# Kernel tuning notes

Hardware: AMD Instinct MI355X
Metric: run time of the kernel (lower is better)

## Reference

```python
import jax, jax.numpy as jnp
import numpy as np

D_MODEL = 1024
NHEAD = 16
HEAD_DIM = D_MODEL // NHEAD
MASK_FILLER = -1e20


def setup_inputs() -> dict:
    key = jax.random.key(0)
    ks = jax.random.split(key, 8)
    B, S = 2, 2048
    query = jax.random.normal(ks[0], (B, S, D_MODEL), dtype=jnp.float32)
    key_t = jax.random.normal(ks[1], (B, S, D_MODEL), dtype=jnp.float32)
    value = jax.random.normal(ks[2], (B, S, D_MODEL), dtype=jnp.float32)
    mask = jax.random.randint(ks[3], (B, S, S), 0, 2, dtype=jnp.int32)
    # nn.Linear(d_model, d_model, bias=False) weights, shape [out, in]
    scale = 1.0 / np.sqrt(D_MODEL)
    wq = jax.random.uniform(ks[4], (D_MODEL, D_MODEL), jnp.float32, -scale, scale)
    wk = jax.random.uniform(ks[5], (D_MODEL, D_MODEL), jnp.float32, -scale, scale)
    wv = jax.random.uniform(ks[6], (D_MODEL, D_MODEL), jnp.float32, -scale, scale)
    wo = jax.random.uniform(ks[7], (D_MODEL, D_MODEL), jnp.float32, -scale, scale)
    return {"query": query, "key": key_t, "value": value, "mask": mask,
            "wq": wq, "wk": wk, "wv": wv, "wo": wo}


def reference(query, key, value, mask, wq, wk, wv, wo):
    B = query.shape[0]
    # Projections: nn.Linear -> x @ W.T
    q = (query @ wq.T).reshape(B, -1, NHEAD, HEAD_DIM).transpose(0, 2, 1, 3)  # [B,H,Sq,Dh]
    k = (key @ wk.T).reshape(B, -1, NHEAD, HEAD_DIM).transpose(0, 2, 1, 3)    # [B,H,Sk,Dh]
    v = (value @ wv.T).reshape(B, -1, NHEAD, HEAD_DIM).transpose(0, 2, 1, 3)  # [B,H,Sk,Dh]
    scores = jnp.einsum('bhqd,bhkd->bhqk', q, k) / jnp.sqrt(jnp.float32(HEAD_DIM))
    scores = jnp.where(mask[:, None, :, :] == 0, MASK_FILLER, scores)
    attn = jax.nn.softmax(scores, axis=-1)  # dropout p=0.0 -> identity
    out = jnp.einsum('bhqk,bhkd->bhqd', attn, v)  # [B,H,Sq,Dh]
    out = out.transpose(0, 2, 1, 3).reshape(B, -1, D_MODEL)
    return out @ wo.T
```

## Files before the change

kernel.cpp:

```cpp
#include <hip/hip_runtime.h>
#include <stdint.h>

typedef __bf16 bf16x8 __attribute__((ext_vector_type(8)));
typedef float floatx4 __attribute__((ext_vector_type(4)));
typedef unsigned short ushort8v __attribute__((ext_vector_type(8)));
typedef unsigned int uint4v __attribute__((ext_vector_type(4)));
typedef unsigned int uint2v __attribute__((ext_vector_type(2)));
typedef unsigned short u16;
typedef unsigned long long u64;

#define GLOAD_LDS16(gp, lp)                                                       \
  __builtin_amdgcn_global_load_lds((__attribute__((address_space(1))) void*)(gp), \
                                   (__attribute__((address_space(3))) void*)(lp), \
                                   16, 0, 0)

__device__ __forceinline__ u16 f2bf(float f) {
  uint32_t u = __builtin_bit_cast(uint32_t, f);
  u = (u + 0x7FFFu + ((u >> 16) & 1u)) >> 16;
  return (u16)u;
}
__device__ __forceinline__ u16 f2bf_up(float f) {
  return (u16)((__builtin_bit_cast(uint32_t, f) + 0x8000u) >> 16);
}

__device__ __forceinline__ ushort8v load8(const void* base, size_t elemOff, int isf32) {
  if (isf32) {
    const uint32_t* p = (const uint32_t*)base + elemOff;
    uint4v a = *(const uint4v*)p;
    uint4v b = *(const uint4v*)(p + 4);
#pragma unroll
    for (int i = 0; i < 4; ++i) { a[i] += 0x8000u; b[i] += 0x8000u; }
    uint4v r;
    r[0] = __builtin_amdgcn_perm(a[1], a[0], 0x07060302);
    r[1] = __builtin_amdgcn_perm(a[3], a[2], 0x07060302);
    r[2] = __builtin_amdgcn_perm(b[1], b[0], 0x07060302);
    r[3] = __builtin_amdgcn_perm(b[3], b[2], 0x07060302);
    return __builtin_bit_cast(ushort8v, r);
  }
  return *(const ushort8v*)((const u16*)base + elemOff);
}

__global__ void detect_dtype(const u16* __restrict__ q, int* __restrict__ flag) {
  if (threadIdx.x == 0) *flag = 0;
  __syncthreads();
  int hit = 0;
  for (int i = threadIdx.x; i < 8192; i += 256) {
    u16 u = q[i];
    if (((u >> 7) & 0xFF) == 0xFF) hit = 1;
  }
  if (hit) atomicOr(flag, 1);
}

__global__ void pack_mask(const int* __restrict__ mask, u64* __restrict__ mpk) {
  const int gw   = (blockIdx.x * 256 + threadIdx.x) >> 6;
  const int lane = threadIdx.x & 63;
  const int word = gw & 31;
  const int row  = gw >> 5;
  const int m = mask[(size_t)row * 2048 + word * 64 + lane];
  u64 bits = __ballot(m != 0);
  if (lane == 0) mpk[(size_t)row * 32 + word] = bits;
}

__global__ __launch_bounds__(256)
void cvt_all(const void* X0, const void* X1, const void* X2,
             const void* W0, const void* W1, const void* W2, const void* W3,
             u16* __restrict__ Xb, u16* __restrict__ Wb, const int* flagp)
{
  const int isf = *flagp;
  const int id = blockIdx.x;
  const int t  = threadIdx.x;
  const int r2  = t >> 7;
  const int col = (t & 127) * 8;
  const void* src; u16* dst; int row;
  if (id < 6144) {
    const int s = id >> 11;
    src = (s == 0) ? X0 : (s == 1) ? X1 : X2;
    row = (id & 2047) * 2 + r2;
    dst = Xb + (size_t)s * 4096 * 1040 + (size_t)row * 1040 + col;
  } else {
    const int s = (id - 6144) >> 9;
    src = (s == 0) ? W0 : (s == 1) ? W1 : (s == 2) ? W2 : W3;
    row = ((id - 6144) & 511) * 2 + r2;
    dst = Wb + (size_t)s * 1024 * 1040 + (size_t)row * 1040 + col;
  }
  *(ushort8v*)dst = load8(src, (size_t)row * 1024 + col, isf);
}

__global__ __launch_bounds__(256)
void cvt_w(const void* W0, const void* W1, const void* W2, const void* W3,
           u16* __restrict__ dst, const int* flagp) {
  const int isf = *flagp;
  const int z = blockIdx.y;
  const void* src = (z == 0) ? W0 : (z == 1) ? W1 : (z == 2) ? W2 : W3;
  const size_t off = ((size_t)blockIdx.x * 256 + threadIdx.x) * 8;
  *(ushort8v*)(dst + (size_t)z * 1024 * 1024 + off) = load8(src, off, isf);
}

__global__ __launch_bounds__(256, 3)
void gemm_qkv_b(const u16* __restrict__ Xb, const u16* __restrict__ Wb,
                u16* __restrict__ Qb, u16* __restrict__ Kb, u16* __restrict__ Vt)
{
  const int AS = 1040, WS = 1040, N = 1024, K = 1024;
  const int z = blockIdx.z;
  const u16* A = Xb + (size_t)z * 4096 * AS;
  const u16* W = Wb + (size_t)z * 1024 * WS;

  __shared__ __align__(16) u16 lA[2 * 128 * 32];
  __shared__ __align__(16) u16 lB[2 * 128 * 32];

  const int tid  = threadIdx.x;
  const int lane = tid & 63;
  const int quad = lane >> 4;
  const int l15  = lane & 15;
  const int w    = tid >> 6;
  const int wm   = w >> 1, wn = w & 1;
  const int tileM = blockIdx.x * 128;
  const int tileN = blockIdx.y * 128;

  floatx4 acc[4][4] = {};

  const int ldRow = tid >> 2;
  const int ldCol = (tid & 3) * 8;
  const u16* aG = A + (size_t)(tileM + ldRow) * AS + ldCol;
  const u16* bG = W + (size_t)(tileN + ldRow) * WS + ldCol;
  u16* lAp = lA + tid * 8;
  u16* lBp = lB + tid * 8;

  GLOAD_LDS16(aG, lAp);
  GLOAD_LDS16(aG + (size_t)64 * AS, lAp + 2048);
  GLOAD_LDS16(bG, lBp);
  GLOAD_LDS16(bG + (size_t)64 * WS, lBp + 2048);
  __syncthreads();

#pragma unroll 2
  for (int k0 = 0; k0 < K; k0 += 32) {
    const int cur = (k0 >> 5) & 1;
    const int nxo = 4096 * (cur ^ 1);
    if (k0 + 32 < K) {
      GLOAD_LDS16(aG + k0 + 32, lAp + nxo);
      GLOAD_LDS16(aG + (size_t)64 * AS + k0 + 32, lAp + nxo + 2048);
      GLOAD_LDS16(bG + k0 + 32, lBp + nxo);
      GLOAD_LDS16(bG + (size_t)64 * WS + k0 + 32, lBp + nxo + 2048);
    }
    const u16* cA = lA + 4096 * cur;
    const u16* cB = lB + 4096 * cur;
    bf16x8 af[4], bw[4];
#pragma unroll
    for (int i = 0; i < 4; ++i) {
      af[i] = *(const bf16x8*)&cA[(wm * 64 + i * 16 + l15) * 32 + quad * 8];
      bw[i] = *(const bf16x8*)&cB[(wn * 64 + i * 16 + l15) * 32 + quad * 8];
    }
#pragma unroll
    for (int i = 0; i < 4; ++i)
#pragma unroll
      for (int j = 0; j < 4; ++j)
        acc[i][j] = __builtin_amdgcn_mfma_f32_16x16x32_bf16(af[i], bw[j], acc[i][j], 0, 0, 0);
    __syncthreads();
  }

  if (z < 2) {
    u16* C = (z == 0) ? Qb : Kb;
    const float sc = (z == 0) ? 0.18033688011112042f : 1.0f;
#pragma unroll
    for (int i = 0; i < 4; ++i) {
      const int row0 = tileM + wm * 64 + i * 16 + quad * 4;
#pragma unroll
      for (int j = 0; j < 4; ++j) {
        const int col = tileN + wn * 64 + j * 16 + l15;
#pragma unroll
        for (int r = 0; r < 4; ++r)
          C[(size_t)(row0 + r) * N + col] = f2bf(acc[i][j][r] * sc);
      }
    }
  } else {
    const int half = w >> 1;
    u16* myT = (w & 1) ? lB : lA;
#pragma unroll
    for (int pass = 0; pass < 2; ++pass) {
      __syncthreads();
      if (half == pass) {
#pragma unroll
        for (int i = 0; i < 4; ++i)
#pragma unroll
          for (int j = 0; j < 4; ++j)
#pragma unroll
            for (int r = 0; r < 4; ++r) {
              const int lr = i * 16 + quad * 4 + r;
              const int lc = j * 16 + l15;
              myT[lr * 64 + (lc ^ (quad << 4))] = f2bf(acc[i][j][r]);
            }
      }
      __syncthreads();
      if (half == pass) {
        const int n    = lane;
        const int gcol = tileN + wn * 64 + n;
        const int hh = gcol >> 6, dd = gcol & 63;
        const int growBase = tileM + wm * 64;
        const int bb = growBase >> 11;
        const int s0 = growBase & 2047;
        u16* dst = Vt + (((size_t)bb * 16 + hh) * 64 + dd) * 2048 + s0;
#pragma unroll
        for (int m0 = 0; m0 < 64; m0 += 8) {
          ushort8v pk;
#pragma unroll
          for (int t = 0; t < 8; ++t) {
            const int m = m0 + t;
            pk[t] = myT[m * 64 + (n ^ ((m & 12) << 2))];
          }
          *(ushort8v*)(dst + m0) = pk;
        }
      }
    }
  }
}

__global__ __launch_bounds__(256)
void gemm_qkv_f(const void* X0, const void* X1, const void* X2,
                const u16* __restrict__ Wb,
                u16* __restrict__ Qb, u16* __restrict__ Kb, u16* __restrict__ Vt,
                const int* flagp)
{
  const int K = 1024, N = 1024;
  const int isf = *flagp;
  const int z = blockIdx.z;
  const void* A_ = (z == 0) ? X0 : (z == 1) ? X1 : X2;
  const u16* W = Wb + (size_t)z * 1024 * 1024;

  __shared__ __align__(16) u16 lA[128 * 32];
  __shared__ __align__(16) u16 lB[128 * 32];

  const int tid  = threadIdx.x;
  const int lane = tid & 63;
  const int quad = lane >> 4;
  const int l15  = lane & 15;
  const int w    = tid >> 6;
  const int wm   = w >> 1, wn = w & 1;
  const int tileM = blockIdx.x * 128;
  const int tileN = blockIdx.y * 128;

  floatx4 acc[4][4] = {};

  const int ldRow = tid >> 2;
  const int ldCol = (tid & 3) * 8;
  const size_t aOff = (size_t)(tileM + ldRow) * K + ldCol;
  const u16* bG = W + (size_t)(tileN + ldRow) * K + ldCol;
  u16* lAp = lA + tid * 8;
  u16* lBp = lB + tid * 8;

  ushort8v a0 = load8(A_, aOff, isf);
  ushort8v a1 = load8(A_, aOff + (size_t)64 * K, isf);
  ushort8v b0 = *(const ushort8v*)bG;
  ushort8v b1 = *(const ushort8v*)(bG + (size_t)64 * K);

  for (int k0 = 0; k0 < K; k0 += 32) {
    __syncthreads();
    *(ushort8v*)lAp          = a0;
    *(ushort8v*)(lAp + 2048) = a1;
    *(ushort8v*)lBp          = b0;
    *(ushort8v*)(lBp + 2048) = b1;
    __syncthreads();

    if (k0 + 32 < K) {
      a0 = load8(A_, aOff + k0 + 32, isf);
      a1 = load8(A_, aOff + (size_t)64 * K + k0 + 32, isf);
      b0 = *(const ushort8v*)(bG + k0 + 32);
      b1 = *(const ushort8v*)(bG + (size_t)64 * K + k0 + 32);
    }

    bf16x8 af[4], bw[4];
#pragma unroll
    for (int i = 0; i < 4; ++i) {
      af[i] = *(const bf16x8*)&lA[(wm * 64 + i * 16 + l15) * 32 + quad * 8];
      bw[i] = *(const bf16x8*)&lB[(wn * 64 + i * 16 + l15) * 32 + quad * 8];
    }
#pragma unroll
    for (int i = 0; i < 4; ++i)
#pragma unroll
      for (int j = 0; j < 4; ++j)
        acc[i][j] = __builtin_amdgcn_mfma_f32_16x16x32_bf16(af[i], bw[j], acc[i][j], 0, 0, 0);
  }

  if (z < 2) {
    u16* C = (z == 0) ? Qb : Kb;
    const float sc = (z == 0) ? 0.18033688011112042f : 1.0f;
#pragma unroll
    for (int i = 0; i < 4; ++i) {
      const int row0 = tileM + wm * 64 + i * 16 + quad * 4;
#pragma unroll
      for (int j = 0; j < 4; ++j) {
        const int col = tileN + wn * 64 + j * 16 + l15;
#pragma unroll
        for (int r = 0; r < 4; ++r)
          C[(size_t)(row0 + r) * N + col] = f2bf(acc[i][j][r] * sc);
      }
    }
  } else {
    const int half = w >> 1;
    u16* myT = (w & 1) ? lB : lA;
#pragma unroll
    for (int pass = 0; pass < 2; ++pass) {
      __syncthreads();
      if (half == pass) {
#pragma unroll
        for (int i = 0; i < 4; ++i)
#pragma unroll
          for (int j = 0; j < 4; ++j)
#pragma unroll
            for (int r = 0; r < 4; ++r) {
              const int lr = i * 16 + quad * 4 + r;
              const int lc = j * 16 + l15;
              myT[lr * 64 + (lc ^ (quad << 4))] = f2bf(acc[i][j][r]);
            }
      }
      __syncthreads();
      if (half == pass) {
        const int n    = lane;
        const int gcol = tileN + wn * 64 + n;
        const int hh = gcol >> 6, dd = gcol & 63;
        const int growBase = tileM + wm * 64;
        const int bb = growBase >> 11;
        const int s0 = growBase & 2047;
        u16* dst = Vt + (((size_t)bb * 16 + hh) * 64 + dd) * 2048 + s0;
#pragma unroll
        for (int m0 = 0; m0 < 64; m0 += 8) {
          ushort8v pk;
#pragma unroll
          for (int t = 0; t < 8; ++t) {
            const int m = m0 + t;
            pk[t] = myT[m * 64 + (n ^ ((m & 12) << 2))];
          }
          *(ushort8v*)(dst + m0) = pk;
        }
      }
    }
  }
}

__global__ __launch_bounds__(256)
void attn(const u16* Qb, const u16* __restrict__ Kb, const u16* __restrict__ Vt,
          const u64* __restrict__ mpk, u16* AO, int aoStr)
{
  __shared__ __align__(16) u16 lK[2][64 * 64];
  __shared__ __align__(16) u16 lV[64 * 64];
  __shared__ __align__(16) u16 lP[4][16 * 64];

  const int tid  = threadIdx.x;
  const int lane = tid & 63;
  const int quad = lane >> 4;
  const int l15  = lane & 15;
  const int w    = tid >> 6;

  const int bh = blockIdx.x;
  const int qt = blockIdx.y;
  const int b  = bh >> 4;
  const int h  = bh & 15;
  const size_t rowB   = (size_t)b * 2048;
  const size_t vtBase = ((size_t)bh * 64) * 2048;

  bf16x8 aq[2];
  {
    const u16* qp = Qb + (rowB + qt * 64 + w * 16 + l15) * 1024 + h * 64 + quad * 8;
    aq[0] = *(const bf16x8*)qp;
    aq[1] = *(const bf16x8*)(qp + 32);
  }

  const ushort8v one_u = {0x3F80, 0x3F80, 0x3F80, 0x3F80, 0x3F80, 0x3F80, 0x3F80, 0x3F80};
  const bf16x8 ones = __builtin_bit_cast(bf16x8, one_u);

  floatx4 o[4], l4;
#pragma unroll
  for (int nb = 0; nb < 4; ++nb) o[nb] = (floatx4){0.f, 0.f, 0.f, 0.f};
  l4 = (floatx4){0.f, 0.f, 0.f, 0.f};

  const u64* mrow = mpk + (rowB + qt * 64 + w * 16 + l15) * 32;
  u16* lPw = &lP[w][0];

  const int r1 = tid >> 3;
  const int cs = ((tid & 7) ^ (r1 & 7)) * 8;
  const u16* kSrc = Kb + (rowB + r1) * 1024 + h * 64 + cs;
  const u16* vSrc = Vt + vtBase + (size_t)r1 * 2048 + cs;

  GLOAD_LDS16(kSrc,                     &lK[0][tid * 8]);
  GLOAD_LDS16(kSrc + (size_t)32 * 1024, &lK[0][tid * 8 + 2048]);

#pragma unroll 2
  for (int kt = 0; kt < 32; ++kt) {
    const int cur = kt & 1;
    __syncthreads();

    {
      const u16* vS = vSrc + kt * 64;
      GLOAD_LDS16(vS,                     &lV[tid * 8]);
      GLOAD_LDS16(vS + (size_t)32 * 2048, &lV[tid * 8 + 2048]);
    }
    if (kt < 31) {
      const u16* kS = kSrc + (size_t)(kt + 1) * 64 * 1024;
      GLOAD_LDS16(kS,                     &lK[cur ^ 1][tid * 8]);
      GLOAD_LDS16(kS + (size_t)32 * 1024, &lK[cur ^ 1][tid * 8 + 2048]);
    }

    const u64 mw = mrow[kt];

#pragma unroll
    for (int nb = 0; nb < 4; ++nb) {
      const int row = nb * 16 + l15;
      const int swk = (row & 7) << 3;
      bf16x8 ak0 = *(const bf16x8*)&lK[cur][row * 64 + ((quad * 8) ^ swk)];
      bf16x8 ak1 = *(const bf16x8*)&lK[cur][row * 64 + ((quad * 8 + 32) ^ swk)];
      floatx4 sacc = {0.f, 0.f, 0.f, 0.f};
      sacc = __builtin_amdgcn_mfma_f32_16x16x32_bf16(ak0, aq[0], sacc, 0, 0, 0);
      sacc = __builtin_amdgcn_mfma_f32_16x16x32_bf16(ak1, aq[1], sacc, 0, 0, 0);
      const uint32_t nib = (uint32_t)(mw >> (nb * 16 + quad * 4)) & 0xFu;
      float p0 = (nib & 1u) ? __builtin_amdgcn_exp2f(sacc[0]) : 0.0f;
      float p1 = (nib & 2u) ? __builtin_amdgcn_exp2f(sacc[1]) : 0.0f;
      float p2 = (nib & 4u) ? __builtin_amdgcn_exp2f(sacc[2]) : 0.0f;
      float p3 = (nib & 8u) ? __builtin_amdgcn_exp2f(sacc[3]) : 0.0f;
      const uint32_t b0 = __builtin_bit_cast(uint32_t, p0) + 0x8000u;
      const uint32_t b1 = __builtin_bit_cast(uint32_t, p1) + 0x8000u;
      const uint32_t b2 = __builtin_bit_cast(uint32_t, p2) + 0x8000u;
      const uint32_t b3 = __builtin_bit_cast(uint32_t, p3) + 0x8000u;
      uint2v pk2;
      pk2[0] = __builtin_amdgcn_perm(b1, b0, 0x07060302);
      pk2[1] = __builtin_amdgcn_perm(b3, b2, 0x07060302);
      const int col = (nb * 16 + quad * 4) ^ ((l15 & 7) << 3);
      *(uint2v*)&lPw[l15 * 64 + col] = pk2;
    }
    __syncthreads();

#pragma unroll
    for (int ks = 0; ks < 2; ++ks) {
      bf16x8 ap = *(const bf16x8*)&lPw[l15 * 64 + ((ks * 32 + quad * 8) ^ ((l15 & 7) << 3))];
#pragma unroll
      for (int nb = 0; nb < 4; ++nb) {
        const int row = nb * 16 + l15;
        bf16x8 bv = *(const bf16x8*)&lV[row * 64 + ((ks * 32 + quad * 8) ^ ((row & 7) << 3))];
        o[nb] = __builtin_amdgcn_mfma_f32_16x16x32_bf16(ap, bv, o[nb], 0, 0, 0);
      }
      l4 = __builtin_amdgcn_mfma_f32_16x16x32_bf16(ap, ones, l4, 0, 0, 0);
    }
  }

#pragma unroll
  for (int r = 0; r < 4; ++r) {
    const float inv = 1.0f / l4[r];
    const size_t orow = (rowB + qt * 64 + w * 16 + quad * 4 + r) * aoStr + h * 64;
#pragma unroll
    for (int nb = 0; nb < 4; ++nb)
      AO[orow + nb * 16 + l15] = f2bf(o[nb][r] * inv);
  }
}

__global__ __launch_bounds__(256, 3)
void gemm_out(const u16* __restrict__ A, int aStr,
              const u16* __restrict__ W, int wStr, void* C_, const int* flagp)
{
  const int K = 1024, N = 1024;
  const int isf = *flagp;

  __shared__ __align__(16) u16 lA[2 * 64 * 32];
  __shared__ __align__(16) u16 lB[2 * 128 * 32];

  const int tid  = threadIdx.x;
  const int lane = tid & 63;
  const int quad = lane >> 4;
  const int l15  = lane & 15;
  const int w    = tid >> 6;
  const int tileM = blockIdx.x * 64;
  const int tileN = blockIdx.y * 128;

  floatx4 acc[4][2] = {};

  const int ldRow = tid >> 2;
  const int ldCol = (tid & 3) * 8;
  const u16* aG = A + (size_t)(tileM + ldRow) * aStr + ldCol;
  const u16* bG = W + (size_t)(tileN + ldRow) * wStr + ldCol;
  u16* lAp = lA + tid * 8;
  u16* lBp = lB + tid * 8;

  GLOAD_LDS16(aG, lAp);
  GLOAD_LDS16(bG, lBp);
  GLOAD_LDS16(bG + (size_t)64 * wStr, lBp + 2048);
  __syncthreads();

#pragma unroll 2
  for (int k0 = 0; k0 < K; k0 += 32) {
    const int cur = (k0 >> 5) & 1;
    const int nxA = 2048 * (cur ^ 1);
    const int nxB = 4096 * (cur ^ 1);
    if (k0 + 32 < K) {
      GLOAD_LDS16(aG + k0 + 32, lAp + nxA);
      GLOAD_LDS16(bG + k0 + 32, lBp + nxB);
      GLOAD_LDS16(bG + (size_t)64 * wStr + k0 + 32, lBp + nxB + 2048);
    }
    const u16* cA = lA + 2048 * cur;
    const u16* cB = lB + 4096 * cur;
    bf16x8 af[4], bw[2];
#pragma unroll
    for (int i = 0; i < 4; ++i)
      af[i] = *(const bf16x8*)&cA[(i * 16 + l15) * 32 + quad * 8];
#pragma unroll
    for (int j = 0; j < 2; ++j)
      bw[j] = *(const bf16x8*)&cB[(w * 32 + j * 16 + l15) * 32 + quad * 8];
#pragma unroll
    for (int i = 0; i < 4; ++i)
#pragma unroll
      for (int j = 0; j < 2; ++j)
        acc[i][j] = __builtin_amdgcn_mfma_f32_16x16x32_bf16(af[i], bw[j], acc[i][j], 0, 0, 0);
    __syncthreads();
  }

#pragma unroll
  for (int i = 0; i < 4; ++i) {
    const int row0 = tileM + i * 16 + quad * 4;
#pragma unroll
    for (int j = 0; j < 2; ++j) {
      const int col = tileN + w * 32 + j * 16 + l15;
#pragma unroll
      for (int r = 0; r < 4; ++r) {
        const size_t off = (size_t)(row0 + r) * N + col;
        if (isf) ((float*)C_)[off] = acc[i][j][r];
        else     ((u16*)C_)[off]   = f2bf(acc[i][j][r]);
      }
    }
  }
}

extern "C" void kernel_launch(void* const* d_in, const int* in_sizes, int n_in,
                              void* d_out, int out_size, void* d_ws, size_t ws_size,
                              hipStream_t stream)
{
  const int* mk = (const int*)d_in[3];

  int* flag = (int*)d_ws;
  u64* mpk  = (u64*)((char*)d_ws + 256);
  const size_t SZ = (size_t)4096 * 1024;
  u16* Qb = (u16*)((char*)d_ws + 256 + (size_t)1048576);
  u16* Kb = Qb + SZ;
  u16* Vt = Kb + SZ;
  u16* Wb = Vt + SZ;

  const size_t WB_PAD = (size_t)4 * 1024 * 1040;
  const size_t XB_PAD = (size_t)3 * 4096 * 1040;
  const size_t NEED = 256 + 1048576 + 3 * SZ * 2 + WB_PAD * 2 + XB_PAD * 2;

  detect_dtype<<<1, 256, 0, stream>>>((const u16*)d_in[0], flag);
  pack_mask<<<32768, 256, 0, stream>>>(mk, mpk);

  if (ws_size >= NEED) {
    u16* Xb = Wb + WB_PAD;
    cvt_all<<<8192, 256, 0, stream>>>(d_in[0], d_in[1], d_in[2],
                                      d_in[4], d_in[5], d_in[6], d_in[7],
                                      Xb, Wb, flag);
    gemm_qkv_b<<<dim3(32, 8, 3), 256, 0, stream>>>(Xb, Wb, Qb, Kb, Vt);
    u16* AOp = Xb;
    attn<<<dim3(32, 32), 256, 0, stream>>>(Qb, Kb, Vt, mpk, AOp, 1040);
    gemm_out<<<dim3(64, 8), 256, 0, stream>>>(AOp, 1040,
                                              Wb + (size_t)3 * 1024 * 1040, 1040,
                                              d_out, flag);
  } else {
    cvt_w<<<dim3(512, 4), 256, 0, stream>>>(d_in[4], d_in[5], d_in[6], d_in[7], Wb, flag);
    gemm_qkv_f<<<dim3(32, 8, 3), 256, 0, stream>>>(d_in[0], d_in[1], d_in[2],
                                                   Wb, Qb, Kb, Vt, flag);
    attn<<<dim3(32, 32), 256, 0, stream>>>(Qb, Kb, Vt, mpk, Qb, 1024);
    gemm_out<<<dim3(64, 8), 256, 0, stream>>>(Qb, 1024,
                                              Wb + (size_t)3 * 1024 * 1024, 1024,
                                              d_out, flag);
  }
}
```

Measured before the change: 280.1 us.

## Double-buffer V tiles, drop mid-loop barrier, and raise MFMA priority in attention

V tiles get a second LDS buffer and are prefetched one iteration ahead alongside K, so the V load overlaps the previous tile's compute. Each wave writes and reads only its own P buffer, so the block-wide barrier between the score and PV phases is removed. MFMA sections are wrapped with s_setprio to favour matrix issue across waves, and P packing switches to native bf16 conversion. The cost is extra LDS per block, which may reduce occupancy, and conversion code that may differ from the previous add-and-permute rounding.

```diff
diff --git a/kernel.cpp b/kernel.cpp
--- a/kernel.cpp
+++ b/kernel.cpp
@@ -2,6 +2,7 @@
 #include <stdint.h>
 
 typedef __bf16 bf16x8 __attribute__((ext_vector_type(8)));
+typedef __bf16 bf16x4 __attribute__((ext_vector_type(4)));
 typedef float floatx4 __attribute__((ext_vector_type(4)));
 typedef unsigned short ushort8v __attribute__((ext_vector_type(8)));
 typedef unsigned int uint4v __attribute__((ext_vector_type(4)));
@@ -18,9 +19,6 @@
   uint32_t u = __builtin_bit_cast(uint32_t, f);
   u = (u + 0x7FFFu + ((u >> 16) & 1u)) >> 16;
   return (u16)u;
-}
-__device__ __forceinline__ u16 f2bf_up(float f) {
-  return (u16)((__builtin_bit_cast(uint32_t, f) + 0x8000u) >> 16);
 }
 
 __device__ __forceinline__ ushort8v load8(const void* base, size_t elemOff, int isf32) {
@@ -341,7 +339,7 @@
           const u64* __restrict__ mpk, u16* AO, int aoStr)
 {
   __shared__ __align__(16) u16 lK[2][64 * 64];
-  __shared__ __align__(16) u16 lV[64 * 64];
+  __shared__ __align__(16) u16 lV[2][64 * 64];
   __shared__ __align__(16) u16 lP[4][16 * 64];
 
   const int tid  = threadIdx.x;
@@ -382,21 +380,20 @@
 
   GLOAD_LDS16(kSrc,                     &lK[0][tid * 8]);
   GLOAD_LDS16(kSrc + (size_t)32 * 1024, &lK[0][tid * 8 + 2048]);
+  GLOAD_LDS16(vSrc,                     &lV[0][tid * 8]);
+  GLOAD_LDS16(vSrc + (size_t)32 * 2048, &lV[0][tid * 8 + 2048]);
 
 #pragma unroll 2
   for (int kt = 0; kt < 32; ++kt) {
     const int cur = kt & 1;
     __syncthreads();
-
-    {
-      const u16* vS = vSrc + kt * 64;
-      GLOAD_LDS16(vS,                     &lV[tid * 8]);
-      GLOAD_LDS16(vS + (size_t)32 * 2048, &lV[tid * 8 + 2048]);
-    }
     if (kt < 31) {
       const u16* kS = kSrc + (size_t)(kt + 1) * 64 * 1024;
+      const u16* vS = vSrc + (kt + 1) * 64;
       GLOAD_LDS16(kS,                     &lK[cur ^ 1][tid * 8]);
       GLOAD_LDS16(kS + (size_t)32 * 1024, &lK[cur ^ 1][tid * 8 + 2048]);
+      GLOAD_LDS16(vS,                     &lV[cur ^ 1][tid * 8]);
+      GLOAD_LDS16(vS + (size_t)32 * 2048, &lV[cur ^ 1][tid * 8 + 2048]);
     }
 
     const u64 mw = mrow[kt];
@@ -408,35 +405,36 @@
       bf16x8 ak0 = *(const bf16x8*)&lK[cur][row * 64 + ((quad * 8) ^ swk)];
       bf16x8 ak1 = *(const bf16x8*)&lK[cur][row * 64 + ((quad * 8 + 32) ^ swk)];
       floatx4 sacc = {0.f, 0.f, 0.f, 0.f};
+      __builtin_amdgcn_s_setprio(1);
       sacc = __builtin_amdgcn_mfma_f32_16x16x32_bf16(ak0, aq[0], sacc, 0, 0, 0);
       sacc = __builtin_amdgcn_mfma_f32_16x16x32_bf16(ak1, aq[1], sacc, 0, 0, 0);
+      __builtin_amdgcn_s_setprio(0);
       const uint32_t nib = (uint32_t)(mw >> (nb * 16 + quad * 4)) & 0xFu;
-      float p0 = (nib & 1u) ? __builtin_amdgcn_exp2f(sacc[0]) : 0.0f;
-      float p1 = (nib & 2u) ? __builtin_amdgcn_exp2f(sacc[1]) : 0.0f;
-      float p2 = (nib & 4u) ? __builtin_amdgcn_exp2f(sacc[2]) : 0.0f;
-      float p3 = (nib & 8u) ? __builtin_amdgcn_exp2f(sacc[3]) : 0.0f;
-      const uint32_t b0 = __builtin_bit_cast(uint32_t, p0) + 0x8000u;
-      const uint32_t b1 = __builtin_bit_cast(uint32_t, p1) + 0x8000u;
-      const uint32_t b2 = __builtin_bit_cast(uint32_t, p2) + 0x8000u;
-      const uint32_t b3 = __builtin_bit_cast(uint32_t, p3) + 0x8000u;
-      uint2v pk2;
-      pk2[0] = __builtin_amdgcn_perm(b1, b0, 0x07060302);
-      pk2[1] = __builtin_amdgcn_perm(b3, b2, 0x07060302);
+      const float p0 = (nib & 1u) ? __builtin_amdgcn_exp2f(sacc[0]) : 0.0f;
+      const float p1 = (nib & 2u) ? __builtin_amdgcn_exp2f(sacc[1]) : 0.0f;
+      const float p2 = (nib & 4u) ? __builtin_amdgcn_exp2f(sacc[2]) : 0.0f;
+      const float p3 = (nib & 8u) ? __builtin_amdgcn_exp2f(sacc[3]) : 0.0f;
+      bf16x4 pk4;
+      pk4[0] = (__bf16)p0; pk4[1] = (__bf16)p1;
+      pk4[2] = (__bf16)p2; pk4[3] = (__bf16)p3;
       const int col = (nb * 16 + quad * 4) ^ ((l15 & 7) << 3);
-      *(uint2v*)&lPw[l15 * 64 + col] = pk2;
-    }
-    __syncthreads();
+      *(bf16x4*)&lPw[l15 * 64 + col] = pk4;
+    }
 
 #pragma unroll
     for (int ks = 0; ks < 2; ++ks) {
       bf16x8 ap = *(const bf16x8*)&lPw[l15 * 64 + ((ks * 32 + quad * 8) ^ ((l15 & 7) << 3))];
-#pragma unroll
-      for (int nb = 0; nb < 4; ++nb) {
-        const int row = nb * 16 + l15;
-        bf16x8 bv = *(const bf16x8*)&lV[row * 64 + ((ks * 32 + quad * 8) ^ ((row & 7) << 3))];
-        o[nb] = __builtin_amdgcn_mfma_f32_16x16x32_bf16(ap, bv, o[nb], 0, 0, 0);
-      }
+      bf16x8 bv0 = *(const bf16x8*)&lV[cur][(0 * 16 + l15) * 64 + ((ks * 32 + quad * 8) ^ ((l15 & 7) << 3))];
+      bf16x8 bv1 = *(const bf16x8*)&lV[cur][(1 * 16 + l15) * 64 + ((ks * 32 + quad * 8) ^ (((16 + l15) & 7) << 3))];
+      bf16x8 bv2 = *(const bf16x8*)&lV[cur][(2 * 16 + l15) * 64 + ((ks * 32 + quad * 8) ^ (((32 + l15) & 7) << 3))];
+      bf16x8 bv3 = *(const bf16x8*)&lV[cur][(3 * 16 + l15) * 64 + ((ks * 32 + quad * 8) ^ (((48 + l15) & 7) << 3))];
+      __builtin_amdgcn_s_setprio(1);
+      o[0] = __builtin_amdgcn_mfma_f32_16x16x32_bf16(ap, bv0, o[0], 0, 0, 0);
+      o[1] = __builtin_amdgcn_mfma_f32_16x16x32_bf16(ap, bv1, o[1], 0, 0, 0);
+      o[2] = __builtin_amdgcn_mfma_f32_16x16x32_bf16(ap, bv2, o[2], 0, 0, 0);
+      o[3] = __builtin_amdgcn_mfma_f32_16x16x32_bf16(ap, bv3, o[3], 0, 0, 0);
       l4 = __builtin_amdgcn_mfma_f32_16x16x32_bf16(ap, ones, l4, 0, 0, 0);
+      __builtin_amdgcn_s_setprio(0);
     }
   }
 
```

New measurement: 279.9 us. Within noise of the previous version (-0.1%).
